# Kernel tuning notes

Hardware: AMD Instinct MI355X
Metric: run time of the kernel (lower is better)

## Reference

```python
import jax, jax.numpy as jnp
import numpy as np

NHEAD = 8

def setup_inputs() -> dict:
    key = jax.random.key(0)
    ks = jax.random.split(key, 6)
    b, n, d = 4, 1024, 512
    emb = jax.random.normal(ks[0], (b, n, d), dtype=jnp.float32)
    dirs = jax.random.normal(ks[1], (b, n, n, 3), dtype=jnp.float32)
    d_mask = jax.random.normal(ks[2], (b * NHEAD, n, n), dtype=jnp.float32) * 0.1
    W_proj = jax.random.normal(ks[3], (d, 3 * d), dtype=jnp.float32) / np.sqrt(d)
    b_proj = jnp.zeros((3 * d,), dtype=jnp.float32)
    w_force = jax.random.normal(ks[4], (d,), dtype=jnp.float32) / np.sqrt(d)
    b_force = jnp.zeros((1,), dtype=jnp.float32)
    return {"emb": emb, "dirs": dirs, "d_mask": d_mask, "W_proj": W_proj,
            "b_proj": b_proj, "w_force": w_force, "b_force": b_force}

def reference(emb, dirs, d_mask, W_proj, b_proj, w_force, b_force):
    b, n, d = emb.shape
    h = NHEAD
    dh = d // h
    scale = jnp.asarray(np.sqrt(d), emb.dtype)
    qkv = emb @ W_proj + b_proj                      # (b,n,3d)
    q, k, v = jnp.split(qkv, 3, axis=-1)
    q = q.reshape(b, n, h, dh).transpose(0, 2, 1, 3) / scale   # (b,h,n,dh)
    k = k.reshape(b, n, h, dh).transpose(0, 2, 1, 3)           # (b,h,n,dh)
    v = v.reshape(b, n, h, dh).transpose(0, 2, 1, 3)           # (b,h,n,dh)
    scores = jnp.einsum('bhid,bhjd->bhij', q, k) + d_mask.reshape(b, h, n, n)
    attn = jax.nn.softmax(scores, axis=-1)                     # (b,h,n,n); dropout in eval mode = identity
    # torch: (attn[...,None] * dirs[:,None]) @ v  materializes (b,h,n,n,3);
    # fused einsum computes the same per-axis weighted sum without it.
    xyz = jnp.einsum('bhij,bija,bhjd->biahd', attn, dirs, v)   # (b,n,3,h,dh)
    xyz = xyz.reshape(b, n, 3, d)
    out = jnp.einsum('bnad,d->bna', xyz, w_force) + b_force[0]  # (b,n,3)
    return out
```

## Files before the change

### kernel.cpp

```cpp
#include <hip/hip_runtime.h>
#include <hip/hip_bf16.h>

#define NH 8
#define BB 4
#define NN 1024
#define DD 512
#define DH 64
#define JSPLIT 4

typedef __bf16 bf16x8 __attribute__((ext_vector_type(8)));
typedef float f32x4 __attribute__((ext_vector_type(4)));

__device__ __forceinline__ unsigned short f2bf(float f) {
    union { float f; unsigned u; } v; v.f = f;
    unsigned u = v.u;
    unsigned r = u + 0x7FFFu + ((u >> 16) & 1u);
    return (unsigned short)(r >> 16);
}

__global__ __launch_bounds__(256) void k_wv(const float* __restrict__ W, const float* __restrict__ w_force,
                                            const float* __restrict__ b_proj, float* __restrict__ wv_eff,
                                            float* __restrict__ s_bias) {
    int wave = threadIdx.x >> 6, lane = threadIdx.x & 63;
    if (blockIdx.x == 128) {
        if (wave == 0) {
            for (int hh = 0; hh < NH; ++hh) {
                float p = b_proj[2 * DD + hh * DH + lane] * w_force[hh * DH + lane];
                for (int off = 32; off; off >>= 1) p += __shfl_xor(p, off);
                if (lane == 0) s_bias[hh] = p;
            }
        }
        return;
    }
    int c = blockIdx.x * 4 + wave;
    const float* wr = W + (size_t)c * (3 * DD) + 2 * DD;
    #pragma unroll
    for (int hh = 0; hh < NH; ++hh) {
        float p = wr[hh * DH + lane] * w_force[hh * DH + lane];
        for (int off = 32; off; off >>= 1) p += __shfl_xor(p, off);
        if (lane == 0) wv_eff[c * 8 + hh] = p;
    }
}

__global__ void k_wt(const float* __restrict__ W, const float* __restrict__ b_proj,
                     unsigned short* __restrict__ Wt, float* __restrict__ bias_eff) {
    __shared__ float tile[32][33];
    int c0 = blockIdx.x * 32;
    int n0 = blockIdx.y * 32;
    int t = threadIdx.x;
    for (int i = 0; i < 4; ++i) {
        int idx = t + i * 256;
        int r = idx >> 5, cn = idx & 31;
        tile[r][cn] = W[(c0 + r) * (3 * DD) + n0 + cn];
    }
    __syncthreads();
    const float rscale = 0.044194173824159216f;
    for (int i = 0; i < 4; ++i) {
        int idx = t + i * 256;
        int nn = idx >> 5, cc = idx & 31;
        float v = tile[cc][nn];
        int n = n0 + nn;
        if (n < DD) v *= rscale;
        Wt[n * DD + c0 + cc] = f2bf(v);
    }
    if (blockIdx.x == 0 && t < 32) {
        int n = n0 + t;
        bias_eff[n] = b_proj[n] * (n < DD ? 0.044194173824159216f : 1.0f);
    }
}

__global__ void k_emb(const float* __restrict__ emb, unsigned short* __restrict__ embb) {
    int t = blockIdx.x * blockDim.x + threadIdx.x;
    float4 v = ((const float4*)emb)[t];
    ushort4 o;
    o.x = f2bf(v.x); o.y = f2bf(v.y); o.z = f2bf(v.z); o.w = f2bf(v.w);
    ((ushort4*)embb)[t] = o;
}

__global__ __launch_bounds__(256) void k_s(const float* __restrict__ emb,
                                           const float* __restrict__ wv_eff,
                                           const float* __restrict__ s_bias,
                                           float* __restrict__ s_ws) {
    int t = blockIdx.x * 256 + threadIdx.x;
    int row = t >> 3;
    int h = t & 7;
    const float* er = emb + (size_t)row * DD;
    const float* wp = wv_eff + h;
    float acc = 0.f;
    #pragma unroll 8
    for (int c4 = 0; c4 < DD / 4; ++c4) {
        float4 e = *(const float4*)(er + c4 * 4);
        acc += e.x * wp[(c4 * 4 + 0) * 8];
        acc += e.y * wp[(c4 * 4 + 1) * 8];
        acc += e.z * wp[(c4 * 4 + 2) * 8];
        acc += e.w * wp[(c4 * 4 + 3) * 8];
    }
    int b = row >> 10, j = row & 1023;
    s_ws[(b * 8 + h) * NN + j] = acc + s_bias[h];
}

__global__ __launch_bounds__(256) void k_gemm(const unsigned short* __restrict__ embb,
                                              const unsigned short* __restrict__ Wt,
                                              const float* __restrict__ bias_eff,
                                              unsigned short* __restrict__ qb,
                                              unsigned short* __restrict__ kb) {
    __shared__ __align__(16) unsigned short a_s[128 * 32];
    __shared__ __align__(16) unsigned short b_s[128 * 32];
    int m0 = blockIdx.x * 128, n0 = blockIdx.y * 128;
    int t = threadIdx.x;
    int wave = t >> 6, lane = t & 63;
    int wr = (wave >> 1) * 64, wc = (wave & 1) * 64;
    int qd = lane >> 4, c = lane & 15;
    int sr = t >> 2, sg = (t & 3) * 8;
    f32x4 acc[4][4] = {};
    for (int k0 = 0; k0 < DD; k0 += 32) {
        uint4 av0 = *(const uint4*)(embb + (size_t)(m0 + sr) * DD + k0 + sg);
        uint4 av1 = *(const uint4*)(embb + (size_t)(m0 + 64 + sr) * DD + k0 + sg);
        uint4 bv0 = *(const uint4*)(Wt + (size_t)(n0 + sr) * DD + k0 + sg);
        uint4 bv1 = *(const uint4*)(Wt + (size_t)(n0 + 64 + sr) * DD + k0 + sg);
        __syncthreads();
        *(uint4*)(&a_s[sr * 32 + sg]) = av0;
        *(uint4*)(&a_s[(64 + sr) * 32 + sg]) = av1;
        *(uint4*)(&b_s[sr * 32 + sg]) = bv0;
        *(uint4*)(&b_s[(64 + sr) * 32 + sg]) = bv1;
        __syncthreads();
        bf16x8 af[4], bfr[4];
        #pragma unroll
        for (int mi = 0; mi < 4; ++mi)
            af[mi] = *(const bf16x8*)(&a_s[(wr + mi * 16 + c) * 32 + qd * 8]);
        #pragma unroll
        for (int ni = 0; ni < 4; ++ni)
            bfr[ni] = *(const bf16x8*)(&b_s[(wc + ni * 16 + c) * 32 + qd * 8]);
        #pragma unroll
        for (int mi = 0; mi < 4; ++mi)
            #pragma unroll
            for (int ni = 0; ni < 4; ++ni)
                acc[mi][ni] = __builtin_amdgcn_mfma_f32_16x16x32_bf16(af[mi], bfr[ni], acc[mi][ni], 0, 0, 0);
    }
    bool isQ = (n0 < DD);
    unsigned short* dst = isQ ? qb : kb;
    int nb = isQ ? n0 : n0 - DD;
    #pragma unroll
    for (int mi = 0; mi < 4; ++mi)
        #pragma unroll
        for (int ni = 0; ni < 4; ++ni) {
            int col = nb + wc + ni * 16 + c;
            float be = bias_eff[isQ ? col : col + DD];
            #pragma unroll
            for (int r = 0; r < 4; ++r) {
                int row = m0 + wr + mi * 16 + qd * 4 + r;
                dst[(size_t)row * DD + col] = f2bf(acc[mi][ni][r] + be);
            }
        }
}

__global__ __launch_bounds__(256) void k_attn(const unsigned short* __restrict__ qb,
                                              const unsigned short* __restrict__ kb,
                                              const float* __restrict__ s_ws,
                                              const float* __restrict__ d_mask,
                                              const float* __restrict__ dirs,
                                              float* __restrict__ part) {
    int blk = blockIdx.x;
    int itile = blk & 63;
    int rest = blk >> 6;
    int hg = rest & 1;
    int b = (rest >> 1) & 3;
    int chunk = rest >> 3;
    int i0 = itile * 16;
    int j_base = chunk * (NN / JSPLIT);
    int t = threadIdx.x;
    int h = hg * 4 + (t >> 6);
    int lane = t & 63, qd = lane >> 4, c = lane & 15;
    int i = i0 + c;

    const unsigned short* qbase = qb + ((size_t)(b * NN + i) * DD + h * DH + qd * 8);
    bf16x8 aq0 = *(const bf16x8*)(qbase);
    bf16x8 aq1 = *(const bf16x8*)(qbase + 32);

    const unsigned short* kp = kb + ((size_t)(b * NN + j_base + c) * DD + h * DH + qd * 8);
    const float* mp = d_mask + (size_t)(b * NH + h) * NN * NN + (size_t)i * NN + j_base + qd * 4;
    const float* sp = s_ws + (b * NH + h) * NN + j_base + qd * 4;
    const float* dp = dirs + (((size_t)b * NN + i) * NN + j_base + qd * 4) * 3;

    float acc0 = 0.f, acc1 = 0.f, acc2 = 0.f, l = 0.f;

    bf16x8 ck0 = *(const bf16x8*)(kp);
    bf16x8 ck1 = *(const bf16x8*)(kp + 32);
    f32x4 cmk = __builtin_nontemporal_load((const f32x4*)mp);
    f32x4 csj = *(const f32x4*)sp;
    f32x4 cd0 = *(const f32x4*)(dp);
    f32x4 cd1 = *(const f32x4*)(dp + 4);
    f32x4 cd2 = *(const f32x4*)(dp + 8);

    auto step = [&](bf16x8 k0, bf16x8 k1, f32x4 mk, f32x4 sj, f32x4 d0, f32x4 d1, f32x4 d2) {
        f32x4 sc = {0.f, 0.f, 0.f, 0.f};
        sc = __builtin_amdgcn_mfma_f32_16x16x32_bf16(k0, aq0, sc, 0, 0, 0);
        sc = __builtin_amdgcn_mfma_f32_16x16x32_bf16(k1, aq1, sc, 0, 0, 0);
        float p0 = __expf(sc[0] + mk.x);
        float p1 = __expf(sc[1] + mk.y);
        float p2 = __expf(sc[2] + mk.z);
        float p3 = __expf(sc[3] + mk.w);
        l += p0 + p1 + p2 + p3;
        float t0 = p0 * sj.x, t1 = p1 * sj.y, t2 = p2 * sj.z, t3 = p3 * sj.w;
        acc0 += t0 * d0.x + t1 * d0.w + t2 * d1.z + t3 * d2.y;
        acc1 += t0 * d0.y + t1 * d1.x + t2 * d1.w + t3 * d2.z;
        acc2 += t0 * d0.z + t1 * d1.y + t2 * d2.x + t3 * d2.w;
    };

    #pragma unroll
    for (int it = 0; it < NN / JSPLIT / 16 - 1; ++it) {
        kp += 16 * DD; mp += 16; sp += 16; dp += 48;
        bf16x8 nk0 = *(const bf16x8*)(kp);
        bf16x8 nk1 = *(const bf16x8*)(kp + 32);
        f32x4 nmk = __builtin_nontemporal_load((const f32x4*)mp);
        f32x4 nsj = *(const f32x4*)sp;
        f32x4 nd0 = *(const f32x4*)(dp);
        f32x4 nd1 = *(const f32x4*)(dp + 4);
        f32x4 nd2 = *(const f32x4*)(dp + 8);
        step(ck0, ck1, cmk, csj, cd0, cd1, cd2);
        ck0 = nk0; ck1 = nk1; cmk = nmk; csj = nsj; cd0 = nd0; cd1 = nd1; cd2 = nd2;
    }
    step(ck0, ck1, cmk, csj, cd0, cd1, cd2);

    l    += __shfl_xor(l, 16);    l    += __shfl_xor(l, 32);
    acc0 += __shfl_xor(acc0, 16); acc0 += __shfl_xor(acc0, 32);
    acc1 += __shfl_xor(acc1, 16); acc1 += __shfl_xor(acc1, 32);
    acc2 += __shfl_xor(acc2, 16); acc2 += __shfl_xor(acc2, 32);
    if (qd == 0) {
        f32x4 o; o[0] = l; o[1] = acc0; o[2] = acc1; o[3] = acc2;
        *(f32x4*)(part + ((((size_t)(chunk * BB + b)) * NH + h) * NN + i) * 4) = o;
    }
}

__global__ __launch_bounds__(256) void k_fin(const float4* __restrict__ part,
                                             const float* __restrict__ b_force,
                                             float* __restrict__ out) {
    int t = blockIdx.x * 256 + threadIdx.x;
    int b = t >> 10, i = t & 1023;
    float o0, o1, o2;
    o0 = o1 = o2 = b_force[0];
    #pragma unroll
    for (int h = 0; h < NH; ++h) {
        float lx = 0.f, a0 = 0.f, a1 = 0.f, a2 = 0.f;
        #pragma unroll
        for (int ch = 0; ch < JSPLIT; ++ch) {
            float4 p = part[(((size_t)(ch * BB + b) * NH + h) * NN) + i];
            lx += p.x; a0 += p.y; a1 += p.z; a2 += p.w;
        }
        float inv = 1.0f / lx;
        o0 += a0 * inv; o1 += a1 * inv; o2 += a2 * inv;
    }
    out[t * 3 + 0] = o0;
    out[t * 3 + 1] = o1;
    out[t * 3 + 2] = o2;
}

extern "C" void kernel_launch(void* const* d_in, const int* in_sizes, int n_in,
                              void* d_out, int out_size, void* d_ws, size_t ws_size,
                              hipStream_t stream) {
    (void)in_sizes; (void)n_in; (void)out_size; (void)ws_size;
    const float* emb     = (const float*)d_in[0];
    const float* dirs    = (const float*)d_in[1];
    const float* d_mask  = (const float*)d_in[2];
    const float* W       = (const float*)d_in[3];
    const float* b_proj  = (const float*)d_in[4];
    const float* w_force = (const float*)d_in[5];
    const float* b_force = (const float*)d_in[6];
    float* out = (float*)d_out;

    char* ws = (char*)d_ws;
    float* wv_eff   = (float*)ws;
    float* s_bias   = wv_eff + 4096;
    float* bias_eff = s_bias + 8;
    float* s_ws     = bias_eff + 1024;
    unsigned short* Wt   = (unsigned short*)(s_ws + 32768);
    unsigned short* embb = Wt + 1024 * 512;
    unsigned short* qb   = embb + 4096 * 512;
    unsigned short* kb   = qb + 4096 * 512;
    float* part = (float*)(kb + 4096 * 512);

    hipLaunchKernelGGL(k_wv,   dim3(129),     dim3(256), 0, stream, W, w_force, b_proj, wv_eff, s_bias);
    hipLaunchKernelGGL(k_wt,   dim3(16, 32),  dim3(256), 0, stream, W, b_proj, Wt, bias_eff);
    hipLaunchKernelGGL(k_emb,  dim3(2048),    dim3(256), 0, stream, emb, embb);
    hipLaunchKernelGGL(k_s,    dim3(128),     dim3(256), 0, stream, emb, wv_eff, s_bias, s_ws);
    hipLaunchKernelGGL(k_gemm, dim3(32, 8),   dim3(256), 0, stream, embb, Wt, bias_eff, qb, kb);
    hipLaunchKernelGGL(k_attn, dim3(BB * 64 * JSPLIT * 2), dim3(256), 0, stream,
                       qb, kb, s_ws, d_mask, dirs, part);
    hipLaunchKernelGGL(k_fin,  dim3(16),      dim3(256), 0, stream, (const float4*)part, b_force, out);
}
```

Measured before the change: 344.0 us.

## Merge prep kernels, fuse emb bf16 cast into GEMM, widen attention blocks

Merges the weight transpose and value-force reduction kernels into one launch. Drops the separate emb-to-bf16 kernel by converting fp32 emb inside the GEMM's global load. Restructures attention so one 512-thread block covers all 8 heads with twice as many j-chunks, which changes the partial layout that k_fin reads. Also halves k_s block size, aiming to cut launch count, an intermediate buffer round trip, and to improve dirs reuse across heads.

```diff
diff --git a/kernel.cpp b/kernel.cpp
--- a/kernel.cpp
+++ b/kernel.cpp
@@ -6,7 +6,7 @@
 #define NN 1024
 #define DD 512
 #define DH 64
-#define JSPLIT 4
+#define JSPLIT 8
 
 typedef __bf16 bf16x8 __attribute__((ext_vector_type(8)));
 typedef float f32x4 __attribute__((ext_vector_type(4)));
@@ -18,11 +18,42 @@
     return (unsigned short)(r >> 16);
 }
 
-__global__ __launch_bounds__(256) void k_wv(const float* __restrict__ W, const float* __restrict__ w_force,
-                                            const float* __restrict__ b_proj, float* __restrict__ wv_eff,
-                                            float* __restrict__ s_bias) {
-    int wave = threadIdx.x >> 6, lane = threadIdx.x & 63;
-    if (blockIdx.x == 128) {
+__global__ __launch_bounds__(256) void k_prep(const float* __restrict__ W,
+                                              const float* __restrict__ b_proj,
+                                              const float* __restrict__ w_force,
+                                              unsigned short* __restrict__ Wt,
+                                              float* __restrict__ bias_eff,
+                                              float* __restrict__ wv_eff,
+                                              float* __restrict__ s_bias) {
+    __shared__ float tile[32][33];
+    int bx = blockIdx.x;
+    int t = threadIdx.x;
+    const float rscale = 0.044194173824159216f;
+    if (bx < 512) {
+        int c0 = (bx & 15) * 32;
+        int n0 = (bx >> 4) * 32;
+        for (int i = 0; i < 4; ++i) {
+            int idx = t + i * 256;
+            int r = idx >> 5, cn = idx & 31;
+            tile[r][cn] = W[(c0 + r) * (3 * DD) + n0 + cn];
+        }
+        __syncthreads();
+        for (int i = 0; i < 4; ++i) {
+            int idx = t + i * 256;
+            int nn = idx >> 5, cc = idx & 31;
+            float v = tile[cc][nn];
+            int n = n0 + nn;
+            if (n < DD) v *= rscale;
+            Wt[n * DD + c0 + cc] = f2bf(v);
+        }
+        if ((bx & 15) == 0 && t < 32) {
+            int n = n0 + t;
+            bias_eff[n] = b_proj[n] * (n < DD ? rscale : 1.0f);
+        }
+        return;
+    }
+    int wave = t >> 6, lane = t & 63;
+    if (bx == 640) {
         if (wave == 0) {
             for (int hh = 0; hh < NH; ++hh) {
                 float p = b_proj[2 * DD + hh * DH + lane] * w_force[hh * DH + lane];
@@ -32,7 +63,7 @@
         }
         return;
     }
-    int c = blockIdx.x * 4 + wave;
+    int c = (bx - 512) * 4 + wave;
     const float* wr = W + (size_t)c * (3 * DD) + 2 * DD;
     #pragma unroll
     for (int hh = 0; hh < NH; ++hh) {
@@ -42,46 +73,11 @@
     }
 }
 
-__global__ void k_wt(const float* __restrict__ W, const float* __restrict__ b_proj,
-                     unsigned short* __restrict__ Wt, float* __restrict__ bias_eff) {
-    __shared__ float tile[32][33];
-    int c0 = blockIdx.x * 32;
-    int n0 = blockIdx.y * 32;
-    int t = threadIdx.x;
-    for (int i = 0; i < 4; ++i) {
-        int idx = t + i * 256;
-        int r = idx >> 5, cn = idx & 31;
-        tile[r][cn] = W[(c0 + r) * (3 * DD) + n0 + cn];
-    }
-    __syncthreads();
-    const float rscale = 0.044194173824159216f;
-    for (int i = 0; i < 4; ++i) {
-        int idx = t + i * 256;
-        int nn = idx >> 5, cc = idx & 31;
-        float v = tile[cc][nn];
-        int n = n0 + nn;
-        if (n < DD) v *= rscale;
-        Wt[n * DD + c0 + cc] = f2bf(v);
-    }
-    if (blockIdx.x == 0 && t < 32) {
-        int n = n0 + t;
-        bias_eff[n] = b_proj[n] * (n < DD ? 0.044194173824159216f : 1.0f);
-    }
-}
-
-__global__ void k_emb(const float* __restrict__ emb, unsigned short* __restrict__ embb) {
-    int t = blockIdx.x * blockDim.x + threadIdx.x;
-    float4 v = ((const float4*)emb)[t];
-    ushort4 o;
-    o.x = f2bf(v.x); o.y = f2bf(v.y); o.z = f2bf(v.z); o.w = f2bf(v.w);
-    ((ushort4*)embb)[t] = o;
-}
-
-__global__ __launch_bounds__(256) void k_s(const float* __restrict__ emb,
+__global__ __launch_bounds__(128) void k_s(const float* __restrict__ emb,
                                            const float* __restrict__ wv_eff,
                                            const float* __restrict__ s_bias,
                                            float* __restrict__ s_ws) {
-    int t = blockIdx.x * 256 + threadIdx.x;
+    int t = blockIdx.x * 128 + threadIdx.x;
     int row = t >> 3;
     int h = t & 7;
     const float* er = emb + (size_t)row * DD;
@@ -99,7 +95,7 @@
     s_ws[(b * 8 + h) * NN + j] = acc + s_bias[h];
 }
 
-__global__ __launch_bounds__(256) void k_gemm(const unsigned short* __restrict__ embb,
+__global__ __launch_bounds__(256) void k_gemm(const float* __restrict__ emb,
                                               const unsigned short* __restrict__ Wt,
                                               const float* __restrict__ bias_eff,
                                               unsigned short* __restrict__ qb,
@@ -114,13 +110,20 @@
     int sr = t >> 2, sg = (t & 3) * 8;
     f32x4 acc[4][4] = {};
     for (int k0 = 0; k0 < DD; k0 += 32) {
-        uint4 av0 = *(const uint4*)(embb + (size_t)(m0 + sr) * DD + k0 + sg);
-        uint4 av1 = *(const uint4*)(embb + (size_t)(m0 + 64 + sr) * DD + k0 + sg);
+        float4 x0 = *(const float4*)(emb + (size_t)(m0 + sr) * DD + k0 + sg);
+        float4 x1 = *(const float4*)(emb + (size_t)(m0 + sr) * DD + k0 + sg + 4);
+        float4 y0 = *(const float4*)(emb + (size_t)(m0 + 64 + sr) * DD + k0 + sg);
+        float4 y1 = *(const float4*)(emb + (size_t)(m0 + 64 + sr) * DD + k0 + sg + 4);
         uint4 bv0 = *(const uint4*)(Wt + (size_t)(n0 + sr) * DD + k0 + sg);
         uint4 bv1 = *(const uint4*)(Wt + (size_t)(n0 + 64 + sr) * DD + k0 + sg);
+        union { unsigned short u[8]; uint4 v; } px, py;
+        px.u[0] = f2bf(x0.x); px.u[1] = f2bf(x0.y); px.u[2] = f2bf(x0.z); px.u[3] = f2bf(x0.w);
+        px.u[4] = f2bf(x1.x); px.u[5] = f2bf(x1.y); px.u[6] = f2bf(x1.z); px.u[7] = f2bf(x1.w);
+        py.u[0] = f2bf(y0.x); py.u[1] = f2bf(y0.y); py.u[2] = f2bf(y0.z); py.u[3] = f2bf(y0.w);
+        py.u[4] = f2bf(y1.x); py.u[5] = f2bf(y1.y); py.u[6] = f2bf(y1.z); py.u[7] = f2bf(y1.w);
         __syncthreads();
-        *(uint4*)(&a_s[sr * 32 + sg]) = av0;
-        *(uint4*)(&a_s[(64 + sr) * 32 + sg]) = av1;
+        *(uint4*)(&a_s[sr * 32 + sg]) = px.v;
+        *(uint4*)(&a_s[(64 + sr) * 32 + sg]) = py.v;
         *(uint4*)(&b_s[sr * 32 + sg]) = bv0;
         *(uint4*)(&b_s[(64 + sr) * 32 + sg]) = bv1;
         __syncthreads();
@@ -154,22 +157,21 @@
         }
 }
 
-__global__ __launch_bounds__(256) void k_attn(const unsigned short* __restrict__ qb,
-                                              const unsigned short* __restrict__ kb,
-                                              const float* __restrict__ s_ws,
-                                              const float* __restrict__ d_mask,
-                                              const float* __restrict__ dirs,
-                                              float* __restrict__ part) {
+__global__ __launch_bounds__(512, 4) void k_attn(const unsigned short* __restrict__ qb,
+                                                 const unsigned short* __restrict__ kb,
+                                                 const float* __restrict__ s_ws,
+                                                 const float* __restrict__ d_mask,
+                                                 const float* __restrict__ dirs,
+                                                 float* __restrict__ part) {
     int blk = blockIdx.x;
     int itile = blk & 63;
     int rest = blk >> 6;
-    int hg = rest & 1;
-    int b = (rest >> 1) & 3;
-    int chunk = rest >> 3;
+    int b = rest & 3;
+    int chunk = rest >> 2;
     int i0 = itile * 16;
     int j_base = chunk * (NN / JSPLIT);
     int t = threadIdx.x;
-    int h = hg * 4 + (t >> 6);
+    int h = t >> 6;
     int lane = t & 63, qd = lane >> 4, c = lane & 15;
     int i = i0 + c;
 
@@ -273,18 +275,16 @@
     float* s_bias   = wv_eff + 4096;
     float* bias_eff = s_bias + 8;
     float* s_ws     = bias_eff + 1024;
-    unsigned short* Wt   = (unsigned short*)(s_ws + 32768);
-    unsigned short* embb = Wt + 1024 * 512;
-    unsigned short* qb   = embb + 4096 * 512;
-    unsigned short* kb   = qb + 4096 * 512;
+    unsigned short* Wt = (unsigned short*)(s_ws + 32768);
+    unsigned short* qb = Wt + 1024 * 512;
+    unsigned short* kb = qb + 4096 * 512;
     float* part = (float*)(kb + 4096 * 512);
 
-    hipLaunchKernelGGL(k_wv,   dim3(129),     dim3(256), 0, stream, W, w_force, b_proj, wv_eff, s_bias);
-    hipLaunchKernelGGL(k_wt,   dim3(16, 32),  dim3(256), 0, stream, W, b_proj, Wt, bias_eff);
-    hipLaunchKernelGGL(k_emb,  dim3(2048),    dim3(256), 0, stream, emb, embb);
-    hipLaunchKernelGGL(k_s,    dim3(128),     dim3(256), 0, stream, emb, wv_eff, s_bias, s_ws);
-    hipLaunchKernelGGL(k_gemm, dim3(32, 8),   dim3(256), 0, stream, embb, Wt, bias_eff, qb, kb);
-    hipLaunchKernelGGL(k_attn, dim3(BB * 64 * JSPLIT * 2), dim3(256), 0, stream,
+    hipLaunchKernelGGL(k_prep, dim3(641),     dim3(256), 0, stream,
+                       W, b_proj, w_force, Wt, bias_eff, wv_eff, s_bias);
+    hipLaunchKernelGGL(k_s,    dim3(256),     dim3(128), 0, stream, emb, wv_eff, s_bias, s_ws);
+    hipLaunchKernelGGL(k_gemm, dim3(32, 8),   dim3(256), 0, stream, emb, Wt, bias_eff, qb, kb);
+    hipLaunchKernelGGL(k_attn, dim3(BB * 64 * JSPLIT), dim3(512), 0, stream,
                        qb, kb, s_ws, d_mask, dirs, part);
     hipLaunchKernelGGL(k_fin,  dim3(16),      dim3(256), 0, stream, (const float4*)part, b_force, out);
 }
```

Result: no change. 345.7 us (+0.5%).
